# Optimization experiments

Hardware: AMD Instinct MI355X
Metric: run time of the kernel (lower is better)

## Reference

```python
import jax, jax.numpy as jnp
import numpy as np

N = 50000
E = 800000
H = 128


def _mlp2(t, w0, w1):
    # two linear layers (no bias), ELU between
    return jax.nn.elu(t @ w0) @ w1


def setup_inputs() -> dict:
    key = jax.random.key(0)
    ks = jax.random.split(key, 6)
    scale = 0.05
    x = jax.random.normal(ks[0], (N, H), dtype=jnp.float32)
    edge_index = jax.random.randint(ks[1], (2, E), 0, N, dtype=jnp.int64)
    w_e0 = jax.random.normal(ks[2], (3 * H, H), dtype=jnp.float32) * scale
    w_e1 = jax.random.normal(ks[3], (H, H), dtype=jnp.float32) * scale
    w_n0 = jax.random.normal(ks[4], (2 * H, H), dtype=jnp.float32) * scale
    w_n1 = jax.random.normal(ks[5], (H, H), dtype=jnp.float32) * scale
    return {"x": x, "edge_index": edge_index,
            "w_e0": w_e0, "w_e1": w_e1, "w_n0": w_n0, "w_n1": w_n1}


def reference(x, edge_index, w_e0, w_e1, w_n0, w_n1):
    src = edge_index[0]  # x_own
    dst = edge_index[1]  # x_nei; messages aggregated at dst (target)
    x_own = x[src]                      # [E, H]
    x_nei = x[dst]                      # [E, H]
    edge_attr = x_own - x_nei           # [E, H]
    feat = jnp.concatenate([x_own, x_nei, edge_attr], axis=1)  # [E, 3H]
    edge_attr = edge_attr + _mlp2(feat, w_e0, w_e1)            # residual edge update
    # scatter-mean of edge features to target nodes (PyG 'mean' aggr)
    agg_sum = jax.ops.segment_sum(edge_attr, dst, num_segments=N)
    cnt = jax.ops.segment_sum(jnp.ones((E,), dtype=x.dtype), dst, num_segments=N)
    edge_agg = agg_sum / jnp.maximum(cnt, 1.0)[:, None]        # [N, H]
    node_feat = jnp.concatenate([x, edge_agg], axis=1)          # [N, 2H]
    return x + _mlp2(node_feat, w_n0, w_n1)
```

## Files before the change

kernel.cpp:

```cpp
#include <hip/hip_runtime.h>
#include <hip/hip_bf16.h>

#define NN 50000
#define NE 800000
#define HD 128
#define NB 391
#define CAP 4096
#define PQ_BLOCKS 391
#define SCAT_BLOCKS ((NE + 8191) / 8192)

typedef unsigned short u16;
typedef unsigned char u8;
typedef unsigned int u32;
typedef __attribute__((ext_vector_type(8))) short short8;
typedef __attribute__((ext_vector_type(4))) float floatx4;
typedef __attribute__((ext_vector_type(2))) float f32x2;
#define MFMA __builtin_amdgcn_mfma_f32_16x16x32_bf16

__device__ __forceinline__ float bf2f(u16 v) {
    union { unsigned int u; float f; } x; x.u = ((unsigned int)v) << 16; return x.f;
}
__device__ __forceinline__ u16 f2bf(float f) {
    union { unsigned int u; float f; } x; x.f = f;
    unsigned int r = x.u + 0x7fff + ((x.u >> 16) & 1);
    return (u16)(r >> 16);
}
__device__ __forceinline__ float elu_fast(float t) {
    return t > 0.f ? t : (__builtin_amdgcn_exp2f(t * 1.44269504088896f) - 1.f);
}
__device__ __forceinline__ u32 pk_fp8(float a, float b) {
    return __builtin_amdgcn_cvt_pk_fp8_f32(a, b, 0u, false);
}

__global__ void k_wb(const float* __restrict__ we0, const float* __restrict__ we1,
                     const float* __restrict__ wn0, const float* __restrict__ wn1,
                     u16* __restrict__ wcombt, u16* __restrict__ we1t,
                     u16* __restrict__ wn0t, u16* __restrict__ wn1t,
                     int* __restrict__ gcursor) {
    int i = blockIdx.x * 256 + threadIdx.x;
    if (i < 32768) {
        int c = i >> 7, k = i & 127;
        float v;
        if (c < 128) v = we0[k * 128 + c] + we0[(256 + k) * 128 + c];
        else { int cc = c - 128; v = we0[(128 + k) * 128 + cc] - we0[(256 + k) * 128 + cc]; }
        wcombt[i] = f2bf(v);
    } else if (i < 49152) {
        int j = i - 32768; int c = j >> 7, k = j & 127;
        we1t[j] = f2bf(we1[k * 128 + c]);
    } else if (i < 81920) {
        int j = i - 49152; int c = j >> 8, k = j & 255;
        wn0t[j] = f2bf(wn0[k * 128 + c]);
    } else if (i < 98304) {
        int j = i - 81920; int c = j >> 7, k = j & 127;
        wn1t[j] = f2bf(wn1[k * 128 + c]);
    } else if (i < 98304 + NB) {
        gcursor[i - 98304] = 0;
    }
}

__global__ __launch_bounds__(256) void k_front(const float* __restrict__ x,
                                               const u16* __restrict__ wcombt,
                                               u8* __restrict__ p8, u16* __restrict__ qb,
                                               u16* __restrict__ xb,
                                               const int* __restrict__ ei,
                                               int* __restrict__ gcursor, u32* __restrict__ ebuf) {
    int tid = threadIdx.x;
    if (blockIdx.x < PQ_BLOCKS) {
        __shared__ u8  pq[128 * 272];
        __shared__ u16 qt[128 * 136];
        int r0 = blockIdx.x * 128;
        int wid = tid >> 6, lane = tid & 63;
        int arow = lane & 15, kblk = lane >> 4;
        int rbase = wid * 32;

        short8 a[2][4];
#pragma unroll
        for (int rt = 0; rt < 2; rt++) {
            int row_local = rbase + rt * 16 + arow;
            int nrow = r0 + row_local; if (nrow >= NN) nrow = NN - 1;
            const float* xrow = &x[(size_t)nrow * 128];
            float4 xf[8];
#pragma unroll
            for (int ks = 0; ks < 4; ks++) {
                xf[2 * ks]     = *(const float4*)&xrow[ks * 32 + kblk * 8];
                xf[2 * ks + 1] = *(const float4*)&xrow[ks * 32 + kblk * 8 + 4];
            }
            const float* xfp = (const float*)xf;
#pragma unroll
            for (int ks = 0; ks < 4; ks++) {
                short8 r;
#pragma unroll
                for (int j = 0; j < 8; j++) r[j] = (short)f2bf(xfp[ks * 8 + j]);
                a[rt][ks] = r;
                *(short8*)&xb[(size_t)nrow * 128 + ks * 32 + kblk * 8] = r;
            }
#pragma unroll
            for (int ks = 0; ks < 4; ks++)
#pragma unroll
                for (int m = 0; m < 4; m++) {
                    u16 v = (u16)pk_fp8(xfp[ks * 8 + 2 * m], xfp[ks * 8 + 2 * m + 1]);
                    *(u16*)&pq[row_local * 272 + 4 * (ks * 16 + kblk * 4 + m) + 2] = v;
                }
        }
        floatx4 acc[2][16];
#pragma unroll
        for (int rt = 0; rt < 2; rt++)
#pragma unroll
            for (int n0 = 0; n0 < 16; n0++) acc[rt][n0] = (floatx4)(0.f);
#pragma unroll
        for (int ks = 0; ks < 4; ks++)
#pragma unroll
            for (int n0 = 0; n0 < 16; n0++) {
                short8 b = *(const short8*)&wcombt[(size_t)(n0 * 16 + arow) * 128 + ks * 32 + kblk * 8];
                acc[0][n0] = MFMA(a[0][ks], b, acc[0][n0], 0, 0, 0);
                acc[1][n0] = MFMA(a[1][ks], b, acc[1][n0], 0, 0, 0);
            }
#pragma unroll
        for (int rt = 0; rt < 2; rt++)
#pragma unroll
            for (int n0 = 0; n0 < 16; n0++)
#pragma unroll
                for (int j = 0; j < 4; j++) {
                    int r = rbase + rt * 16 + kblk * 4 + j;
                    int col = n0 * 16 + arow;
                    float v = acc[rt][n0][j];
                    if (n0 < 8) pq[r * 272 + 4 * (col >> 1) + (col & 1)] = (u8)pk_fp8(v, v);
                    else        qt[r * 136 + (col - 128)] = f2bf(v);
                }
        __syncthreads();
        for (int s = tid; s < 128 * 16; s += 256) {
            int r = s >> 4, cb = (s & 15) * 16;
            int n = r0 + r;
            if (n < NN) *(short8*)&p8[(size_t)n * 256 + cb] = *(const short8*)&pq[r * 272 + cb];
        }
        for (int s = tid; s < 128 * 16; s += 256) {
            int r = s >> 4, cb = (s & 15) * 8;
            int n = r0 + r;
            if (n < NN) *(short8*)&qb[(size_t)n * 128 + cb] = *(const short8*)&qt[r * 136 + cb];
        }
    } else {
        __shared__ int lh[NB], lbase[NB], lrank[NB];
        int bs = (blockIdx.x - PQ_BLOCKS) * 8192;
        for (int t = tid; t < NB; t += 256) { lh[t] = 0; lrank[t] = 0; }
        __syncthreads();
        int srcv[32], dstv[32];
#pragma unroll
        for (int k = 0; k < 8; k++) {
            int e = bs + k * 1024 + tid * 4;
            int4 s4, d4;
            if (e < NE) { s4 = *(const int4*)&ei[e]; d4 = *(const int4*)&ei[NE + e]; }
            else { s4 = make_int4(0, 0, 0, 0); d4 = make_int4(-1, -1, -1, -1); }
            srcv[4 * k + 0] = s4.x; srcv[4 * k + 1] = s4.y; srcv[4 * k + 2] = s4.z; srcv[4 * k + 3] = s4.w;
            dstv[4 * k + 0] = d4.x; dstv[4 * k + 1] = d4.y; dstv[4 * k + 2] = d4.z; dstv[4 * k + 3] = d4.w;
        }
#pragma unroll
        for (int i = 0; i < 32; i++)
            if (dstv[i] >= 0) atomicAdd(&lh[dstv[i] >> 7], 1);
        __syncthreads();
        for (int t = tid; t < NB; t += 256)
            if (lh[t]) lbase[t] = atomicAdd(&gcursor[t], lh[t]);
        __syncthreads();
#pragma unroll
        for (int i = 0; i < 32; i++) {
            int d = dstv[i];
            if (d >= 0) {
                int b = d >> 7;
                int r = atomicAdd(&lrank[b], 1);
                ebuf[(size_t)b * CAP + lbase[b] + r] = (u32)srcv[i] | ((u32)(d & 127) << 16);
            }
        }
    }
}

__global__ __launch_bounds__(256) void k_bsort(const u32* __restrict__ ebuf,
                                               const int* __restrict__ gcursor,
                                               int* __restrict__ obeg, int* __restrict__ oend,
                                               int* __restrict__ srcs) {
    __shared__ int hist[128], excl[128], cur[128];
    int bb = blockIdx.x;
    int tid = threadIdx.x;
    int beg = bb * CAP;
    int cnt = gcursor[bb];
    int end = beg + cnt;
    if (tid < 128) hist[tid] = 0;
    __syncthreads();
    for (int s = beg + tid; s < end; s += 256)
        atomicAdd(&hist[(ebuf[s] >> 16) & 127], 1);
    __syncthreads();
    if (tid == 0) {
        int run = 0;
        for (int i = 0; i < 128; i++) { excl[i] = run; run += hist[i]; }
    }
    __syncthreads();
    int nodebase = bb * 128;
    if (tid < 128) {
        cur[tid] = beg + excl[tid];
        int n = nodebase + tid;
        if (n < NN) {
            obeg[n] = beg + excl[tid];
            oend[n] = beg + excl[tid] + hist[tid];
        }
    }
    if (tid == 0) {
#pragma unroll
        for (int k = 0; k < 8; k++) srcs[end + k] = 0;
    }
    __syncthreads();
    for (int s = beg + tid; s < end; s += 256) {
        u32 pe = ebuf[s];
        int dl = (pe >> 16) & 127;
        int pos = atomicAdd(&cur[dl], 1);
        srcs[pos] = (int)(pe & 0xFFFF);
    }
}

__global__ __launch_bounds__(256) void k_agg(const u8* __restrict__ p8, const u16* __restrict__ qb,
                                             const u16* __restrict__ xb,
                                             const int* __restrict__ obeg, const int* __restrict__ oend,
                                             const int* __restrict__ srcs,
                                             u16* __restrict__ esumx) {
    const u32* p8r = (const u32*)p8;
    int wave = threadIdx.x >> 6, lane = threadIdx.x & 63;
    int n = blockIdx.x * 4 + wave;
    if (n >= NN) return;
    int beg = obeg[n], end = oend[n];
    ushort2 qv = *(const ushort2*)(qb + (size_t)n * 128 + 2 * lane);
    float q0 = bf2f(qv.x), q1 = bf2f(qv.y);
    float e0 = 0.f, e1 = 0.f, s0 = 0.f, s1 = 0.f;
    int s = beg;
    if (end > beg) {
        int sr[8];
#pragma unroll
        for (int j = 0; j < 8; j++) sr[j] = srcs[beg + j];
        for (; s + 8 <= end; s += 8) {
            u32 d[8];
#pragma unroll
            for (int j = 0; j < 8; j++) d[j] = p8r[((u32)sr[j] << 6) + (u32)lane];
            int nb = s + 8;
            if (nb < end) {
#pragma unroll
                for (int j = 0; j < 8; j++) sr[j] = srcs[nb + j];
            }
#pragma unroll
            for (int j = 0; j < 8; j++) {
                f32x2 pp = __builtin_amdgcn_cvt_pk_f32_fp8(d[j], false);
                f32x2 xp = __builtin_amdgcn_cvt_pk_f32_fp8(d[j], true);
                e0 += elu_fast(pp[0] + q0);
                e1 += elu_fast(pp[1] + q1);
                s0 += xp[0]; s1 += xp[1];
            }
        }
        if (s < end) {
            u32 d[8];
#pragma unroll
            for (int j = 0; j < 8; j++) d[j] = p8r[((u32)sr[j] << 6) + (u32)lane];
#pragma unroll
            for (int j = 0; j < 8; j++) {
                bool live = (s + j < end);
                f32x2 pp = __builtin_amdgcn_cvt_pk_f32_fp8(d[j], false);
                f32x2 xp = __builtin_amdgcn_cvt_pk_f32_fp8(d[j], true);
                float c0 = elu_fast(pp[0] + q0), c1 = elu_fast(pp[1] + q1);
                e0 += live ? c0 : 0.f;
                e1 += live ? c1 : 0.f;
                s0 += live ? xp[0] : 0.f;
                s1 += live ? xp[1] : 0.f;
            }
        }
    }
    float cntf = (float)(end - beg);
    float inv = 1.f / fmaxf(cntf, 1.f);
    ushort2 xo = *(const ushort2*)(xb + (size_t)n * 128 + 2 * lane);
    s0 = (s0 - cntf * bf2f(xo.x)) * inv;
    s1 = (s1 - cntf * bf2f(xo.y)) * inv;
    e0 *= inv; e1 *= inv;
    ushort2 oe = { f2bf(e0), f2bf(e1) };
    ushort2 os = { f2bf(s0), f2bf(s1) };
    *(ushort2*)(esumx + (size_t)n * 256 + 2 * lane) = oe;
    *(ushort2*)(esumx + (size_t)n * 256 + 128 + 2 * lane) = os;
}

__global__ __launch_bounds__(256, 2) void k_node_mfma(const float* __restrict__ x,
                                                      const u16* __restrict__ xb,
                                                      const u16* __restrict__ esumx,
                                                      const u16* __restrict__ we1t,
                                                      const u16* __restrict__ wn0t,
                                                      const u16* __restrict__ wn1t,
                                                      float* __restrict__ out) {
    __shared__ u16 tile[128 * 136];
    int r0 = blockIdx.x * 128;
    int tid = threadIdx.x, wid = tid >> 6, lane = tid & 63;
    int arow = lane & 15, kblk = lane >> 4;
    int rbase = wid * 32;
    int nrow[2];
#pragma unroll
    for (int rt = 0; rt < 2; rt++) {
        int n = r0 + rbase + rt * 16 + arow; if (n >= NN) n = NN - 1;
        nrow[rt] = n;
    }
    short8 stg[8];
#pragma unroll
    for (int t = 0; t < 8; t++) {
        int idx = t * 64 + lane;
        int r = idx >> 4, cb = (idx & 15) * 8;
        int n = r0 + rbase + r; if (n >= NN) n = NN - 1;
        stg[t] = *(const short8*)&esumx[(size_t)n * 256 + 128 + cb];
    }
    short8 a1[2][4], ax[2][4];
#pragma unroll
    for (int rt = 0; rt < 2; rt++)
#pragma unroll
        for (int ks = 0; ks < 4; ks++) {
            a1[rt][ks] = *(const short8*)&esumx[(size_t)nrow[rt] * 256 + ks * 32 + kblk * 8];
            ax[rt][ks] = *(const short8*)&xb[(size_t)nrow[rt] * 128 + ks * 32 + kblk * 8];
        }
#pragma unroll
    for (int t = 0; t < 8; t++) {
        int idx = t * 64 + lane;
        int r = rbase + (idx >> 4), cb = (idx & 15) * 8;
        *(short8*)&tile[r * 136 + cb] = stg[t];
    }
    floatx4 acc[2][8];
#pragma unroll
    for (int rt = 0; rt < 2; rt++)
#pragma unroll
        for (int n0 = 0; n0 < 8; n0++) acc[rt][n0] = (floatx4)(0.f);
#pragma unroll
    for (int ks = 0; ks < 4; ks++)
#pragma unroll
        for (int n0 = 0; n0 < 8; n0++) {
            short8 b = *(const short8*)&we1t[(size_t)(n0 * 16 + arow) * 128 + ks * 32 + kblk * 8];
            acc[0][n0] = MFMA(a1[0][ks], b, acc[0][n0], 0, 0, 0);
            acc[1][n0] = MFMA(a1[1][ks], b, acc[1][n0], 0, 0, 0);
        }
#pragma unroll
    for (int rt = 0; rt < 2; rt++)
#pragma unroll
        for (int n0 = 0; n0 < 8; n0++)
#pragma unroll
            for (int j = 0; j < 4; j++) {
                int rloc = rbase + rt * 16 + kblk * 4 + j;
                int col = n0 * 16 + arow;
                float m = acc[rt][n0][j] + bf2f(tile[rloc * 136 + col]);
                tile[rloc * 136 + col] = f2bf(m);
            }
#pragma unroll
    for (int rt = 0; rt < 2; rt++)
#pragma unroll
        for (int n0 = 0; n0 < 8; n0++) acc[rt][n0] = (floatx4)(0.f);
#pragma unroll
    for (int ks = 0; ks < 4; ks++) {
        short8 am[2];
#pragma unroll
        for (int rt = 0; rt < 2; rt++)
            am[rt] = *(const short8*)&tile[(rbase + rt * 16 + arow) * 136 + ks * 32 + kblk * 8];
#pragma unroll
        for (int n0 = 0; n0 < 8; n0++) {
            short8 bx = *(const short8*)&wn0t[(size_t)(n0 * 16 + arow) * 256 + ks * 32 + kblk * 8];
            short8 bm = *(const short8*)&wn0t[(size_t)(n0 * 16 + arow) * 256 + 128 + ks * 32 + kblk * 8];
#pragma unroll
            for (int rt = 0; rt < 2; rt++) {
                acc[rt][n0] = MFMA(ax[rt][ks], bx, acc[rt][n0], 0, 0, 0);
                acc[rt][n0] = MFMA(am[rt], bm, acc[rt][n0], 0, 0, 0);
            }
        }
    }
#pragma unroll
    for (int rt = 0; rt < 2; rt++)
#pragma unroll
        for (int n0 = 0; n0 < 8; n0++)
#pragma unroll
            for (int j = 0; j < 4; j++) {
                int rloc = rbase + rt * 16 + kblk * 4 + j;
                tile[rloc * 136 + n0 * 16 + arow] = f2bf(elu_fast(acc[rt][n0][j]));
            }
#pragma unroll
    for (int rt = 0; rt < 2; rt++)
#pragma unroll
        for (int n0 = 0; n0 < 8; n0++) acc[rt][n0] = (floatx4)(0.f);
#pragma unroll
    for (int ks = 0; ks < 4; ks++) {
        short8 a[2];
#pragma unroll
        for (int rt = 0; rt < 2; rt++)
            a[rt] = *(const short8*)&tile[(rbase + rt * 16 + arow) * 136 + ks * 32 + kblk * 8];
#pragma unroll
        for (int n0 = 0; n0 < 8; n0++) {
            short8 b = *(const short8*)&wn1t[(size_t)(n0 * 16 + arow) * 128 + ks * 32 + kblk * 8];
            acc[0][n0] = MFMA(a[0], b, acc[0][n0], 0, 0, 0);
            acc[1][n0] = MFMA(a[1], b, acc[1][n0], 0, 0, 0);
        }
    }
#pragma unroll
    for (int rt = 0; rt < 2; rt++)
#pragma unroll
        for (int n0 = 0; n0 < 8; n0++)
#pragma unroll
            for (int j = 0; j < 4; j++)
                tile[(rbase + rt * 16 + kblk * 4 + j) * 136 + n0 * 16 + arow] = f2bf(acc[rt][n0][j]);
#pragma unroll
    for (int t = 0; t < 16; t++) {
        int idx = t * 64 + lane;
        int r = idx >> 5, cb = (idx & 31) * 4;
        int n = r0 + rbase + r;
        if (n < NN) {
            float4 xv = *(const float4*)&x[(size_t)n * 128 + cb];
            ushort4 tv = *(const ushort4*)&tile[(rbase + r) * 136 + cb];
            float4 o = { xv.x + bf2f(tv.x), xv.y + bf2f(tv.y), xv.z + bf2f(tv.z), xv.w + bf2f(tv.w) };
            *(float4*)&out[(size_t)n * 128 + cb] = o;
        }
    }
}

extern "C" void kernel_launch(void* const* d_in, const int* in_sizes, int n_in,
                              void* d_out, int out_size, void* d_ws, size_t ws_size,
                              hipStream_t stream) {
    const float* x       = (const float*)d_in[0];
    const int* ei        = (const int*)d_in[1];
    const float* we0     = (const float*)d_in[2];
    const float* we1     = (const float*)d_in[3];
    const float* wn0     = (const float*)d_in[4];
    const float* wn1     = (const float*)d_in[5];
    float* out           = (float*)d_out;

    char* w = (char*)d_ws;
    size_t off = 0;
    auto alloc = [&](size_t bytes) -> void* {
        off = (off + 255) & ~(size_t)255;
        void* p = w + off;
        off += bytes;
        return p;
    };
    u16*   wcombt = (u16*)alloc(256 * 128 * sizeof(u16));
    u16*   we1t   = (u16*)alloc(128 * 128 * sizeof(u16));
    u16*   wn0t   = (u16*)alloc(128 * 256 * sizeof(u16));
    u16*   wn1t   = (u16*)alloc(128 * 128 * sizeof(u16));
    u8*    p8     = (u8*)alloc((size_t)NN * 256 * sizeof(u8));
    u16*   qb     = (u16*)alloc((size_t)NN * 128 * sizeof(u16));
    u16*   xb     = (u16*)alloc((size_t)NN * 128 * sizeof(u16));
    u16*   esumx  = (u16*)alloc((size_t)NN * 256 * sizeof(u16));
    int*   gcursor= (int*)alloc(NB * sizeof(int));
    u32*   ebuf   = (u32*)alloc((size_t)NB * CAP * sizeof(u32));
    int*   obeg   = (int*)alloc((size_t)NN * sizeof(int));
    int*   oend   = (int*)alloc((size_t)NN * sizeof(int));
    int*   srcs   = (int*)alloc(((size_t)NB * CAP + 64) * sizeof(int));
    (void)ws_size; (void)in_sizes; (void)n_in; (void)out_size;

    k_wb<<<(98304 + NB + 255) / 256, 256, 0, stream>>>(we0, we1, wn0, wn1,
                                                       wcombt, we1t, wn0t, wn1t, gcursor);
    k_front<<<PQ_BLOCKS + SCAT_BLOCKS, 256, 0, stream>>>(x, wcombt, p8, qb, xb,
                                                         ei, gcursor, ebuf);
    k_bsort<<<NB, 256, 0, stream>>>(ebuf, gcursor, obeg, oend, srcs);
    k_agg<<<(NN + 3) / 4, 256, 0, stream>>>(p8, qb, xb, obeg, oend, srcs, esumx);
    k_node_mfma<<<(NN + 127) / 128, 256, 0, stream>>>(x, xb, esumx, we1t, wn0t, wn1t, out);
}
```

Before: 141.9 us.

## Fuse bucket sort and neighbor aggregation into one kernel with LDS source lists

Merges the per-bucket counting sort and the per-node gather/aggregate into a single 1024-thread kernel per 128-node bucket. Sorted source indices stay in LDS instead of being written to and re-read from global srcs/obeg/oend arrays, and one kernel launch is removed. The serial prefix scan is replaced by a parallel Hillis-Steele scan. In exchange, only 391 large blocks run the gather phase, with each wave handling 8 nodes in sequence. This may lower occupancy and latency hiding compared with the previous 12500-block aggregation kernel.

```diff
diff --git a/kernel.cpp b/kernel.cpp
--- a/kernel.cpp
+++ b/kernel.cpp
@@ -172,111 +172,109 @@
     }
 }
 
-__global__ __launch_bounds__(256) void k_bsort(const u32* __restrict__ ebuf,
-                                               const int* __restrict__ gcursor,
-                                               int* __restrict__ obeg, int* __restrict__ oend,
-                                               int* __restrict__ srcs) {
-    __shared__ int hist[128], excl[128], cur[128];
+__global__ __launch_bounds__(1024) void k_sortagg(const u8* __restrict__ p8,
+                                                  const u16* __restrict__ qb,
+                                                  const u16* __restrict__ xb,
+                                                  const int* __restrict__ gcursor,
+                                                  const u32* __restrict__ ebuf,
+                                                  u16* __restrict__ esumx) {
+    __shared__ int hist[128], scan[128], cur[128];
+    __shared__ u32 lsrc[CAP + 8];
+    const u32* p8r = (const u32*)p8;
     int bb = blockIdx.x;
     int tid = threadIdx.x;
     int beg = bb * CAP;
     int cnt = gcursor[bb];
-    int end = beg + cnt;
+    int nodebase = bb * 128;
+
     if (tid < 128) hist[tid] = 0;
     __syncthreads();
-    for (int s = beg + tid; s < end; s += 256)
-        atomicAdd(&hist[(ebuf[s] >> 16) & 127], 1);
+    for (int s = tid; s < cnt; s += 1024)
+        atomicAdd(&hist[(ebuf[beg + s] >> 16) & 127], 1);
     __syncthreads();
-    if (tid == 0) {
-        int run = 0;
-        for (int i = 0; i < 128; i++) { excl[i] = run; run += hist[i]; }
-    }
+    if (tid < 128) scan[tid] = hist[tid];
     __syncthreads();
-    int nodebase = bb * 128;
-    if (tid < 128) {
-        cur[tid] = beg + excl[tid];
-        int n = nodebase + tid;
-        if (n < NN) {
-            obeg[n] = beg + excl[tid];
-            oend[n] = beg + excl[tid] + hist[tid];
-        }
-    }
-    if (tid == 0) {
-#pragma unroll
-        for (int k = 0; k < 8; k++) srcs[end + k] = 0;
-    }
+#pragma unroll
+    for (int off = 1; off < 128; off <<= 1) {
+        int v = (tid < 128 && tid >= off) ? scan[tid - off] : 0;
+        __syncthreads();
+        if (tid < 128) scan[tid] += v;
+        __syncthreads();
+    }
+    if (tid < 128) cur[tid] = scan[tid] - hist[tid];
+    if (tid < 8) lsrc[cnt + tid] = 0;
     __syncthreads();
-    for (int s = beg + tid; s < end; s += 256) {
-        u32 pe = ebuf[s];
+    for (int s = tid; s < cnt; s += 1024) {
+        u32 pe = ebuf[beg + s];
         int dl = (pe >> 16) & 127;
         int pos = atomicAdd(&cur[dl], 1);
-        srcs[pos] = (int)(pe & 0xFFFF);
-    }
-}
-
-__global__ __launch_bounds__(256) void k_agg(const u8* __restrict__ p8, const u16* __restrict__ qb,
-                                             const u16* __restrict__ xb,
-                                             const int* __restrict__ obeg, const int* __restrict__ oend,
-                                             const int* __restrict__ srcs,
-                                             u16* __restrict__ esumx) {
-    const u32* p8r = (const u32*)p8;
-    int wave = threadIdx.x >> 6, lane = threadIdx.x & 63;
-    int n = blockIdx.x * 4 + wave;
-    if (n >= NN) return;
-    int beg = obeg[n], end = oend[n];
-    ushort2 qv = *(const ushort2*)(qb + (size_t)n * 128 + 2 * lane);
-    float q0 = bf2f(qv.x), q1 = bf2f(qv.y);
-    float e0 = 0.f, e1 = 0.f, s0 = 0.f, s1 = 0.f;
-    int s = beg;
-    if (end > beg) {
-        int sr[8];
-#pragma unroll
-        for (int j = 0; j < 8; j++) sr[j] = srcs[beg + j];
-        for (; s + 8 <= end; s += 8) {
-            u32 d[8];
-#pragma unroll
-            for (int j = 0; j < 8; j++) d[j] = p8r[((u32)sr[j] << 6) + (u32)lane];
-            int nb = s + 8;
-            if (nb < end) {
-#pragma unroll
-                for (int j = 0; j < 8; j++) sr[j] = srcs[nb + j];
-            }
-#pragma unroll
-            for (int j = 0; j < 8; j++) {
-                f32x2 pp = __builtin_amdgcn_cvt_pk_f32_fp8(d[j], false);
-                f32x2 xp = __builtin_amdgcn_cvt_pk_f32_fp8(d[j], true);
-                e0 += elu_fast(pp[0] + q0);
-                e1 += elu_fast(pp[1] + q1);
-                s0 += xp[0]; s1 += xp[1];
-            }
-        }
-        if (s < end) {
-            u32 d[8];
-#pragma unroll
-            for (int j = 0; j < 8; j++) d[j] = p8r[((u32)sr[j] << 6) + (u32)lane];
-#pragma unroll
-            for (int j = 0; j < 8; j++) {
-                bool live = (s + j < end);
-                f32x2 pp = __builtin_amdgcn_cvt_pk_f32_fp8(d[j], false);
-                f32x2 xp = __builtin_amdgcn_cvt_pk_f32_fp8(d[j], true);
-                float c0 = elu_fast(pp[0] + q0), c1 = elu_fast(pp[1] + q1);
-                e0 += live ? c0 : 0.f;
-                e1 += live ? c1 : 0.f;
-                s0 += live ? xp[0] : 0.f;
-                s1 += live ? xp[1] : 0.f;
-            }
-        }
-    }
-    float cntf = (float)(end - beg);
-    float inv = 1.f / fmaxf(cntf, 1.f);
-    ushort2 xo = *(const ushort2*)(xb + (size_t)n * 128 + 2 * lane);
-    s0 = (s0 - cntf * bf2f(xo.x)) * inv;
-    s1 = (s1 - cntf * bf2f(xo.y)) * inv;
-    e0 *= inv; e1 *= inv;
-    ushort2 oe = { f2bf(e0), f2bf(e1) };
-    ushort2 os = { f2bf(s0), f2bf(s1) };
-    *(ushort2*)(esumx + (size_t)n * 256 + 2 * lane) = oe;
-    *(ushort2*)(esumx + (size_t)n * 256 + 128 + 2 * lane) = os;
+        lsrc[pos] = pe & 0xFFFF;
+    }
+    __syncthreads();
+
+    int wave = tid >> 6, lane = tid & 63;
+#pragma unroll
+    for (int i = 0; i < 8; i++) {
+        int dl = wave * 8 + i;
+        int n = nodebase + dl;
+        if (n >= NN) continue;
+        int nb_ = scan[dl];
+        int na_ = nb_ - hist[dl];
+        int deg = nb_ - na_;
+        ushort2 qv = *(const ushort2*)(qb + (size_t)n * 128 + 2 * lane);
+        float q0 = bf2f(qv.x), q1 = bf2f(qv.y);
+        float e0 = 0.f, e1 = 0.f, s0 = 0.f, s1 = 0.f;
+        int s = na_;
+        if (deg > 0) {
+            u32 sr[8];
+#pragma unroll
+            for (int j = 0; j < 8; j++) sr[j] = lsrc[na_ + j];
+            for (; s + 8 <= nb_; s += 8) {
+                u32 d[8];
+#pragma unroll
+                for (int j = 0; j < 8; j++) d[j] = p8r[(sr[j] << 6) + (u32)lane];
+                int nxt = s + 8;
+                if (nxt < nb_) {
+#pragma unroll
+                    for (int j = 0; j < 8; j++) sr[j] = lsrc[nxt + j];
+                }
+#pragma unroll
+                for (int j = 0; j < 8; j++) {
+                    f32x2 pp = __builtin_amdgcn_cvt_pk_f32_fp8(d[j], false);
+                    f32x2 xp = __builtin_amdgcn_cvt_pk_f32_fp8(d[j], true);
+                    e0 += elu_fast(pp[0] + q0);
+                    e1 += elu_fast(pp[1] + q1);
+                    s0 += xp[0]; s1 += xp[1];
+                }
+            }
+            if (s < nb_) {
+                u32 d[8];
+#pragma unroll
+                for (int j = 0; j < 8; j++) d[j] = p8r[(sr[j] << 6) + (u32)lane];
+#pragma unroll
+                for (int j = 0; j < 8; j++) {
+                    bool live = (s + j < nb_);
+                    f32x2 pp = __builtin_amdgcn_cvt_pk_f32_fp8(d[j], false);
+                    f32x2 xp = __builtin_amdgcn_cvt_pk_f32_fp8(d[j], true);
+                    float c0 = elu_fast(pp[0] + q0), c1 = elu_fast(pp[1] + q1);
+                    e0 += live ? c0 : 0.f;
+                    e1 += live ? c1 : 0.f;
+                    s0 += live ? xp[0] : 0.f;
+                    s1 += live ? xp[1] : 0.f;
+                }
+            }
+        }
+        float cntf = (float)deg;
+        float inv = 1.f / fmaxf(cntf, 1.f);
+        ushort2 xo = *(const ushort2*)(xb + (size_t)n * 128 + 2 * lane);
+        s0 = (s0 - cntf * bf2f(xo.x)) * inv;
+        s1 = (s1 - cntf * bf2f(xo.y)) * inv;
+        e0 *= inv; e1 *= inv;
+        ushort2 oe = { f2bf(e0), f2bf(e1) };
+        ushort2 os = { f2bf(s0), f2bf(s1) };
+        *(ushort2*)(esumx + (size_t)n * 256 + 2 * lane) = oe;
+        *(ushort2*)(esumx + (size_t)n * 256 + 128 + 2 * lane) = os;
+    }
 }
 
 __global__ __launch_bounds__(256, 2) void k_node_mfma(const float* __restrict__ x,
@@ -440,16 +438,12 @@
     u16*   esumx  = (u16*)alloc((size_t)NN * 256 * sizeof(u16));
     int*   gcursor= (int*)alloc(NB * sizeof(int));
     u32*   ebuf   = (u32*)alloc((size_t)NB * CAP * sizeof(u32));
-    int*   obeg   = (int*)alloc((size_t)NN * sizeof(int));
-    int*   oend   = (int*)alloc((size_t)NN * sizeof(int));
-    int*   srcs   = (int*)alloc(((size_t)NB * CAP + 64) * sizeof(int));
     (void)ws_size; (void)in_sizes; (void)n_in; (void)out_size;
 
     k_wb<<<(98304 + NB + 255) / 256, 256, 0, stream>>>(we0, we1, wn0, wn1,
                                                        wcombt, we1t, wn0t, wn1t, gcursor);
     k_front<<<PQ_BLOCKS + SCAT_BLOCKS, 256, 0, stream>>>(x, wcombt, p8, qb, xb,
                                                          ei, gcursor, ebuf);
-    k_bsort<<<NB, 256, 0, stream>>>(ebuf, gcursor, obeg, oend, srcs);
-    k_agg<<<(NN + 3) / 4, 256, 0, stream>>>(p8, qb, xb, obeg, oend, srcs, esumx);
+    k_sortagg<<<NB, 1024, 0, stream>>>(p8, qb, xb, gcursor, ebuf, esumx);
     k_node_mfma<<<(NN + 127) / 128, 256, 0, stream>>>(x, xb, esumx, we1t, wn0t, wn1t, out);
 }
```

Result: slower. 154.7 us (+9.0%).
